# Kernel optimization log

Hardware: AMD Instinct MI355X
Metric: run time of the kernel (lower is better)

Reference implementation:

```python
import jax, jax.numpy as jnp
import numpy as np

B, S, D = 4, 2048, 1024
E = 16          # num_experts
K = 2           # num_experts_per_tok
F = 512         # moe_intermediate_size
FS = 2048       # shared_expert_intermediate_size


def setup_inputs() -> dict:
    key = jax.random.key(0)
    ks = jax.random.split(key, 9)
    s = 0.02
    return {
        "hidden_states": jax.random.normal(ks[0], (B, S, D), jnp.float32),
        "router_w": jax.random.normal(ks[1], (E, D), jnp.float32) * s,   # torch Linear-style [out,in]
        "Wg": jax.random.normal(ks[2], (E, D, F), jnp.float32) * s,      # gate_proj per expert
        "Wu": jax.random.normal(ks[3], (E, D, F), jnp.float32) * s,      # up_proj per expert
        "Wd": jax.random.normal(ks[4], (E, F, D), jnp.float32) * s,      # down_proj per expert
        "Sg": jax.random.normal(ks[5], (D, FS), jnp.float32) * s,        # shared expert gate_proj
        "Su": jax.random.normal(ks[6], (D, FS), jnp.float32) * s,        # shared expert up_proj
        "Sd": jax.random.normal(ks[7], (FS, D), jnp.float32) * s,        # shared expert down_proj
        "shared_gate_w": jax.random.normal(ks[8], (D, 1), jnp.float32) * s,
    }


def reference(hidden_states, router_w, Wg, Wu, Wd, Sg, Su, Sd, shared_gate_w):
    b, s, d = hidden_states.shape
    x = hidden_states.reshape(-1, d)                      # [T, D]
    T = x.shape[0]

    # --- router (Qwen3NextTopKRouter): fp32 softmax -> topk -> renorm ---
    logits = jnp.einsum("td,ed->te", x.astype(jnp.float32), router_w.astype(jnp.float32))
    probs = jax.nn.softmax(logits, axis=-1)               # [T, E]
    top_w, top_i = jax.lax.top_k(probs, K)                # [T, K]
    top_w = top_w / jnp.sum(top_w, axis=-1, keepdims=True)  # norm_topk_prob
    top_w = top_w.astype(x.dtype)

    # dense combine weights [T, E]: zero except at selected experts (index_add semantics)
    dense_w = jnp.zeros((T, E), x.dtype).at[jnp.arange(T)[:, None], top_i].add(top_w)

    # --- experts: SwiGLU per expert, scan over the fixed expert axis ---
    def body(acc, params):
        wg, wu, wd, cw = params                            # cw: [T]
        h = jax.nn.silu(x @ wg) * (x @ wu)                 # [T, F]
        return acc + cw[:, None] * (h @ wd), None

    expert_out, _ = jax.lax.scan(body, jnp.zeros_like(x), (Wg, Wu, Wd, dense_w.T))

    # --- shared expert with sigmoid gate ---
    shared = (jax.nn.silu(x @ Sg) * (x @ Su)) @ Sd         # [T, D]
    shared = jax.nn.sigmoid(x @ shared_gate_w) * shared

    out = expert_out + shared
    return out.reshape(b, s, d)
```

## Files before the change

kernel.cpp:

```cpp
#include <hip/hip_runtime.h>

typedef __attribute__((ext_vector_type(8))) short short8;
typedef __attribute__((ext_vector_type(4))) float f32x4;
typedef unsigned short u16;
typedef unsigned int u32;

#define DEVI __device__ __forceinline__

DEVI u16 f2b(float f) {
  u32 u = __float_as_uint(f);
  u32 r = u + 0x7FFFu + ((u >> 16) & 1u);
  return (u16)(r >> 16);
}
DEVI float b2f(u16 h) { return __uint_as_float(((u32)h) << 16); }
DEVI float silu(float g) { return g / (1.f + __expf(-g)); }

constexpr int T_ = 8192, D_ = 1024, E_ = 16, F_ = 512, FS_ = 2048;

constexpr size_t OFF_XB   = 0;
constexpr size_t OFF_WGU  = OFF_XB  + (size_t)T_ * D_ * 2;
constexpr size_t OFF_WDT  = OFF_WGU + (size_t)E_ * 2 * F_ * D_ * 2;
constexpr size_t OFF_SGU  = OFF_WDT + (size_t)E_ * D_ * F_ * 2;
constexpr size_t OFF_SDT  = OFF_SGU + (size_t)2 * FS_ * D_ * 2;
constexpr size_t OFF_HB   = OFF_SDT + (size_t)D_ * FS_ * 2;
constexpr size_t OFF_HS   = OFF_HB  + (size_t)2 * T_ * F_ * 2;
constexpr size_t OFF_PAIR = OFF_HS  + (size_t)T_ * FS_ * 2;
constexpr size_t OFF_PW   = OFF_PAIR + (size_t)2 * T_ * D_ * 2;
constexpr size_t OFF_GATE = OFF_PW  + (size_t)2 * T_ * 4;
constexpr size_t OFF_CNT  = OFF_GATE + (size_t)T_ * 4;
constexpr size_t OFF_TOP2 = OFF_CNT + 64;
constexpr size_t OFF_LIST = OFF_TOP2 + (size_t)T_ * 4;

__global__ void prep_kernel(
    const float4* __restrict__ x4, const float4* __restrict__ rw4,
    const float4* __restrict__ sgw4, int* __restrict__ top2e,
    float* __restrict__ pw, float* __restrict__ gate, ushort4* __restrict__ xb4,
    const float* __restrict__ Wg, const float* __restrict__ Wu, const float* __restrict__ Wd,
    const float* __restrict__ Sg, const float* __restrict__ Su, const float* __restrict__ Sd,
    u16* __restrict__ wgu, u16* __restrict__ wdT,
    u16* __restrict__ sgu, u16* __restrict__ sdT) {
  const int tid = threadIdx.x;
  const int bid = blockIdx.x;
  if (bid >= 7680) {
    const int lane = tid & 63, wid = tid >> 6;
    const int t = (bid - 7680) * 4 + wid;
    const float4* xr = x4 + (size_t)t * (D_ / 4);
    float acc[17];
#pragma unroll
    for (int e = 0; e < 17; ++e) acc[e] = 0.f;
    ushort4 xo[4];
#pragma unroll
    for (int j = 0; j < 4; ++j) {
      const int d4 = j * 64 + lane;
      float4 xv = xr[d4];
      xo[j] = make_ushort4(f2b(xv.x), f2b(xv.y), f2b(xv.z), f2b(xv.w));
#pragma unroll
      for (int e = 0; e < 16; ++e) {
        float4 wv = rw4[e * 256 + d4];
        acc[e] = fmaf(xv.x, wv.x, fmaf(xv.y, wv.y, fmaf(xv.z, wv.z, fmaf(xv.w, wv.w, acc[e]))));
      }
      float4 sv = sgw4[d4];
      acc[16] = fmaf(xv.x, sv.x, fmaf(xv.y, sv.y, fmaf(xv.z, sv.z, fmaf(xv.w, sv.w, acc[16]))));
    }
#pragma unroll
    for (int j = 0; j < 4; ++j)
      xb4[(size_t)t * 256 + j * 64 + lane] = xo[j];
#pragma unroll
    for (int e = 0; e < 17; ++e) {
      float v = acc[e];
#pragma unroll
      for (int off = 32; off; off >>= 1) v += __shfl_xor(v, off);
      acc[e] = v;
    }
    if (lane == 0) {
      int i1 = 0; float l1 = acc[0];
#pragma unroll
      for (int e = 1; e < 16; ++e) if (acc[e] > l1) { l1 = acc[e]; i1 = e; }
      int i2 = (i1 == 0) ? 1 : 0; float l2 = acc[i2];
#pragma unroll
      for (int e = 0; e < 16; ++e) {
        if (e == i1) continue;
        if (acc[e] > l2) { l2 = acc[e]; i2 = e; }
      }
      float w1 = 1.f / (1.f + expf(l2 - l1));
      top2e[t] = i1 | (i2 << 8);
      pw[2 * t] = w1;
      pw[2 * t + 1] = 1.f - w1;
      gate[t] = 1.f / (1.f + expf(-acc[16]));
    }
    return;
  }
  __shared__ float lds[64][65];
  int i = bid;
  const float* in; u16* out; int R, C, mode, rem;
  if (i < 6144) {
    int j = i >> 11; rem = i & 2047;
    int b = rem >> 7; rem &= 127;
    if (j == 0)      { in = Wg + (size_t)b * D_ * F_; out = wgu + (size_t)b * 2 * F_ * D_; R = D_; C = F_;  mode = 0; }
    else if (j == 1) { in = Wu + (size_t)b * D_ * F_; out = wgu + (size_t)b * 2 * F_ * D_; R = D_; C = F_;  mode = 1; }
    else             { in = Wd + (size_t)b * F_ * D_; out = wdT + (size_t)b * D_ * F_;     R = F_; C = D_;  mode = 2; }
  } else {
    int r2 = i - 6144; int j = r2 >> 9; rem = r2 & 511;
    if (j == 0)      { in = Sg; out = sgu; R = D_;  C = FS_; mode = 0; }
    else if (j == 1) { in = Su; out = sgu; R = D_;  C = FS_; mode = 1; }
    else             { in = Sd; out = sdT; R = FS_; C = D_;  mode = 2; }
  }
  const int ntx = C >> 6;
  const int cx = rem % ntx, cy = rem / ntx;
  const int c0 = cx * 64, r0 = cy * 64;
  {
    const int tx4 = (tid & 15) * 4, ty = tid >> 4;
#pragma unroll
    for (int p = 0; p < 4; ++p) {
      const int rr = ty + p * 16;
      float4 v = *(const float4*)&in[(size_t)(r0 + rr) * C + c0 + tx4];
      lds[rr][tx4] = v.x; lds[rr][tx4 + 1] = v.y; lds[rr][tx4 + 2] = v.z; lds[rr][tx4 + 3] = v.w;
    }
  }
  __syncthreads();
  {
    const int ol = tid >> 2, seg = tid & 3;
    const int f = c0 + ol;
    size_t orow;
    if (mode == 2) orow = f;
    else orow = (size_t)((f >> 4) << 5) + (f & 15) + (mode == 1 ? 16 : 0);
    u16 vals[16];
#pragma unroll
    for (int k = 0; k < 16; ++k) vals[k] = f2b(lds[seg * 16 + k][ol]);
    u16* dst = out + orow * R + r0 + seg * 16;
    *(short8*)dst = *(short8*)&vals[0];
    *(short8*)(dst + 8) = *(short8*)&vals[8];
  }
}

__global__ __launch_bounds__(1024) void compact_kernel(
    const int* __restrict__ top2e, int* __restrict__ lists, int* __restrict__ counts) {
  const int e = blockIdx.x;
  const int tid = threadIdx.x, lane = tid & 63, wid = tid >> 6;
  __shared__ int wsum[16];
  __shared__ int base;
  if (tid == 0) base = 0;
  __syncthreads();
  for (int c0 = 0; c0 < T_; c0 += 1024) {
    const int t = c0 + tid;
    const int pk = top2e[t];
    int slot = -1;
    if ((pk & 0xFF) == e) slot = 2 * t;
    else if (((pk >> 8) & 0xFF) == e) slot = 2 * t + 1;
    const unsigned long long m = __ballot(slot >= 0);
    const int myofs = __popcll(m & ((1ULL << lane) - 1ULL));
    if (lane == 0) wsum[wid] = __popcll(m);
    __syncthreads();
    const int b = base;
    int wbase = 0;
#pragma unroll
    for (int w = 0; w < 16; ++w) if (w < wid) wbase += wsum[w];
    if (slot >= 0) lists[e * T_ + b + wbase + myofs] = slot;
    __syncthreads();
    if (tid == 0) {
      int s = 0;
#pragma unroll
      for (int w = 0; w < 16; ++w) s += wsum[w];
      base += s;
    }
    __syncthreads();
  }
  if (tid == 0) counts[e] = base;
}

DEVI void gl_lds16(const void* gsrc, void* lds) {
  __builtin_amdgcn_global_load_lds((const __attribute__((address_space(1))) unsigned int*)gsrc,
                                   (__attribute__((address_space(3))) unsigned int*)lds, 16, 0, 0);
}

DEVI void prefix16(const int* counts, int e, int& cnt, int& roff) {
  cnt = counts[e];
  int s = 0;
#pragma unroll
  for (int k = 0; k < E_; ++k) s += (k < e) ? counts[k] : 0;
  roff = s;
}

__global__ __launch_bounds__(256, 2) void gu_gemm(
    const u16* __restrict__ xb, const u16* __restrict__ wgu, const u16* __restrict__ sgu,
    u16* __restrict__ hb, u16* __restrict__ hs,
    const int* __restrict__ counts, const int* __restrict__ lists) {
  extern __shared__ char smem[];
  const int tid = threadIdx.x;
  const int bid = blockIdx.x;
  const bool se = (bid >= 2048);
  int mt, nt, e = 0, cnt = 0, roff = 0;
  const u16* B0;
  if (!se) {
    e = bid >> 7; int r = bid & 127; mt = r >> 3; nt = r & 7;
    prefix16(counts, e, cnt, roff);
    if (mt * 128 >= cnt) return;
    B0 = wgu + (size_t)e * 2 * F_ * D_;
  } else {
    int st = bid - 2048;
    mt = st & 63; nt = st >> 6;
    B0 = sgu;
  }

  const int lane = tid & 63, wid = tid >> 6;
  const int wm = wid >> 1, wn = wid & 1;
  const int lr = lane & 15, lg = lane >> 4;
  const int ldsrow = tid >> 3;
  const int kslot = (tid & 7) << 4;
  constexpr size_t strideB = (size_t)D_ * 2;
  const char* aSrc[4]; const char* bSrc[4];
#pragma unroll
  for (int q = 0; q < 4; ++q) {
    int row = q * 32 + ldsrow;
    int kb = kslot ^ ((row & 7) << 4);
    int r = mt * 128 + row;
    long arow;
    if (!se) arow = (r < cnt) ? (lists[e * T_ + r] >> 1) : 0;
    else arow = r;
    aSrc[q] = (const char*)xb + (size_t)arow * strideB + kb;
    int nrow = nt * 128 + row;
    bSrc[q] = (const char*)B0 + (size_t)nrow * strideB + kb;
  }

  const f32x4 fz = {0.f, 0.f, 0.f, 0.f};
  f32x4 acc[4][4];
#pragma unroll
  for (int i = 0; i < 4; ++i)
#pragma unroll
    for (int j = 0; j < 4; ++j) acc[i][j] = fz;

  const int sw = (lr & 7) << 4;
  constexpr int nks = D_ / 64;

  {
    char* dst = smem;
#pragma unroll
    for (int q = 0; q < 4; ++q) gl_lds16(aSrc[q], dst + q * 4096 + tid * 16);
#pragma unroll
    for (int q = 0; q < 4; ++q) gl_lds16(bSrc[q], dst + 16384 + q * 4096 + tid * 16);
  }
  __syncthreads();

  int cur = 0;
  for (int ks = 0; ks < nks; ++ks) {
    if (ks + 1 < nks) {
      const int kbo = (ks + 1) * 128;
      char* dst = smem + (cur ^ 1) * 32768;
#pragma unroll
      for (int q = 0; q < 4; ++q) gl_lds16(aSrc[q] + kbo, dst + q * 4096 + tid * 16);
#pragma unroll
      for (int q = 0; q < 4; ++q) gl_lds16(bSrc[q] + kbo, dst + 16384 + q * 4096 + tid * 16);
    }
    const char* As = smem + cur * 32768;
    const char* Bs = As + 16384;
#pragma unroll
    for (int kk = 0; kk < 2; ++kk) {
      const int ko = kk * 64 + lg * 16;
      short8 af[4];
#pragma unroll
      for (int fm = 0; fm < 4; ++fm) {
        int row = wm * 64 + fm * 16 + lr;
        af[fm] = *(const short8*)(As + row * 128 + (ko ^ sw));
      }
#pragma unroll
      for (int fn = 0; fn < 4; ++fn) {
        int col = wn * 64 + fn * 16 + lr;
        short8 bf = *(const short8*)(Bs + col * 128 + (ko ^ sw));
#pragma unroll
        for (int fm = 0; fm < 4; ++fm)
          acc[fm][fn] = __builtin_amdgcn_mfma_f32_16x16x32_bf16(af[fm], bf, acc[fm][fn], 0, 0, 0);
      }
    }
    __syncthreads();
    cur ^= 1;
  }

  const int c0 = 16 * (4 * nt + 2 * wn);
  const int r0 = mt * 128;
#pragma unroll
  for (int fm = 0; fm < 4; ++fm) {
#pragma unroll
    for (int j = 0; j < 4; ++j) {
      const int r = r0 + wm * 64 + fm * 16 + lg * 4 + j;
      if (!se && r >= cnt) continue;
      float h0 = silu(acc[fm][0][j]) * acc[fm][1][j];
      float h1 = silu(acc[fm][2][j]) * acc[fm][3][j];
      if (!se) {
        hb[(size_t)(roff + r) * F_ + c0 + lr] = f2b(h0);
        hb[(size_t)(roff + r) * F_ + c0 + 16 + lr] = f2b(h1);
      } else {
        hs[(size_t)r * FS_ + c0 + lr] = f2b(h0);
        hs[(size_t)r * FS_ + c0 + 16 + lr] = f2b(h1);
      }
    }
  }
}

template <int MODE>
__global__ __launch_bounds__(256, 2) void moe_gemm(
    const u16* __restrict__ Abase, const u16* __restrict__ B0,
    u16* __restrict__ outb, float* __restrict__ outf,
    const int* __restrict__ counts, const int* __restrict__ lists,
    const float* __restrict__ pw, const float* __restrict__ gate,
    const u16* __restrict__ pairb, int Kdim) {
  extern __shared__ char smem[];
  const int tid = threadIdx.x;
  const int mt = blockIdx.x, nt = blockIdx.y, e = blockIdx.z;

  int cnt = 0;
  const u16* A = Abase;
  if constexpr (MODE == 1) {
    int roff;
    prefix16(counts, e, cnt, roff);
    if (mt * 128 >= cnt) return;
    A = Abase + (size_t)roff * Kdim;
    B0 += (size_t)e * D_ * F_;
  }

  const int lane = tid & 63, wid = tid >> 6;
  const int wm = wid >> 1, wn = wid & 1;
  const int lr = lane & 15, lg = lane >> 4;
  const int ldsrow = tid >> 3;
  const int kslot = (tid & 7) << 4;
  const size_t strideB = (size_t)Kdim * 2;
  const char* aSrc[4]; const char* bSrc[4];
#pragma unroll
  for (int q = 0; q < 4; ++q) {
    int row = q * 32 + ldsrow;
    int kb = kslot ^ ((row & 7) << 4);
    long arow;
    if constexpr (MODE == 1) {
      int r = mt * 128 + row;
      arow = (r < cnt) ? r : (cnt - 1);
    } else {
      arow = mt * 128 + row;
    }
    aSrc[q] = (const char*)A + (size_t)arow * strideB + kb;
    int nrow = nt * 128 + row;
    bSrc[q] = (const char*)B0 + (size_t)nrow * strideB + kb;
  }

  const f32x4 fz = {0.f, 0.f, 0.f, 0.f};
  f32x4 acc[4][4];
#pragma unroll
  for (int i = 0; i < 4; ++i)
#pragma unroll
    for (int j = 0; j < 4; ++j) acc[i][j] = fz;

  const int nks = Kdim >> 6;
  const int sw = (lr & 7) << 4;

  {
    char* dst = smem;
#pragma unroll
    for (int q = 0; q < 4; ++q) gl_lds16(aSrc[q], dst + q * 4096 + tid * 16);
#pragma unroll
    for (int q = 0; q < 4; ++q) gl_lds16(bSrc[q], dst + 16384 + q * 4096 + tid * 16);
  }
  __syncthreads();

  int cur = 0;
  for (int ks = 0; ks < nks; ++ks) {
    if (ks + 1 < nks) {
      const int kbo = (ks + 1) * 128;
      char* dst = smem + (cur ^ 1) * 32768;
#pragma unroll
      for (int q = 0; q < 4; ++q) gl_lds16(aSrc[q] + kbo, dst + q * 4096 + tid * 16);
#pragma unroll
      for (int q = 0; q < 4; ++q) gl_lds16(bSrc[q] + kbo, dst + 16384 + q * 4096 + tid * 16);
    }
    const char* As = smem + cur * 32768;
    const char* Bs = As + 16384;
#pragma unroll
    for (int kk = 0; kk < 2; ++kk) {
      const int ko = kk * 64 + lg * 16;
      short8 af[4];
#pragma unroll
      for (int fm = 0; fm < 4; ++fm) {
        int row = wm * 64 + fm * 16 + lr;
        af[fm] = *(const short8*)(As + row * 128 + (ko ^ sw));
      }
#pragma unroll
      for (int fn = 0; fn < 4; ++fn) {
        int col = wn * 64 + fn * 16 + lr;
        short8 bf = *(const short8*)(Bs + col * 128 + (ko ^ sw));
#pragma unroll
        for (int fm = 0; fm < 4; ++fm)
          acc[fm][fn] = __builtin_amdgcn_mfma_f32_16x16x32_bf16(af[fm], bf, acc[fm][fn], 0, 0, 0);
      }
    }
    __syncthreads();
    cur ^= 1;
  }

  const int r0 = mt * 128;
#pragma unroll
  for (int fm = 0; fm < 4; ++fm) {
#pragma unroll
    for (int j = 0; j < 4; ++j) {
      const int rowt = wm * 64 + fm * 16 + lg * 4 + j;
      const int r = r0 + rowt;
      if constexpr (MODE == 1) {
        if (r >= cnt) continue;
      }
      int slot = 0;
      float rsc = 0.f;
      if constexpr (MODE == 1) { slot = lists[e * T_ + r]; rsc = pw[slot]; }
      if constexpr (MODE == 3) rsc = gate[r];
#pragma unroll
      for (int fn = 0; fn < 4; ++fn) {
        const int c = nt * 128 + wn * 64 + fn * 16 + lr;
        float v = acc[fm][fn][j];
        if constexpr (MODE == 1) {
          outb[(size_t)slot * D_ + c] = f2b(rsc * v);
        } else {
          float o = v * rsc + b2f(pairb[(size_t)(2 * r) * D_ + c]) + b2f(pairb[(size_t)(2 * r + 1) * D_ + c]);
          outf[(size_t)r * D_ + c] = o;
        }
      }
    }
  }
}

extern "C" void kernel_launch(void* const* d_in, const int* in_sizes, int n_in,
                              void* d_out, int out_size, void* d_ws, size_t ws_size,
                              hipStream_t stream) {
  const float* x   = (const float*)d_in[0];
  const float* rw  = (const float*)d_in[1];
  const float* Wg  = (const float*)d_in[2];
  const float* Wu  = (const float*)d_in[3];
  const float* Wd  = (const float*)d_in[4];
  const float* Sg  = (const float*)d_in[5];
  const float* Su  = (const float*)d_in[6];
  const float* Sd  = (const float*)d_in[7];
  const float* sgw = (const float*)d_in[8];
  float* out = (float*)d_out;

  unsigned char* ws = (unsigned char*)d_ws;
  u16* xb    = (u16*)(ws + OFF_XB);
  u16* wgu   = (u16*)(ws + OFF_WGU);
  u16* wdT   = (u16*)(ws + OFF_WDT);
  u16* sgu   = (u16*)(ws + OFF_SGU);
  u16* sdT   = (u16*)(ws + OFF_SDT);
  u16* hb    = (u16*)(ws + OFF_HB);
  u16* hs    = (u16*)(ws + OFF_HS);
  u16* pairb = (u16*)(ws + OFF_PAIR);
  float* pwf   = (float*)(ws + OFF_PW);
  float* gatef = (float*)(ws + OFF_GATE);
  int* cnti    = (int*)(ws + OFF_CNT);
  int* top2i   = (int*)(ws + OFF_TOP2);
  int* listsi  = (int*)(ws + OFF_LIST);

  prep_kernel<<<9728, 256, 0, stream>>>(
      (const float4*)x, (const float4*)rw, (const float4*)sgw,
      top2i, pwf, gatef, (ushort4*)xb,
      Wg, Wu, Wd, Sg, Su, Sd, wgu, wdT, sgu, sdT);
  compact_kernel<<<E_, 1024, 0, stream>>>(top2i, listsi, cnti);

  gu_gemm<<<4096, 256, 65536, stream>>>(xb, wgu, sgu, hb, hs, cnti, listsi);
  moe_gemm<1><<<dim3(16, 8, 16), 256, 65536, stream>>>(hb, wdT, pairb, nullptr,
                                                       cnti, listsi, pwf, gatef, nullptr, 512);
  moe_gemm<3><<<dim3(64, 8, 1), 256, 65536, stream>>>(hs, sdT, nullptr, out,
                                                      cnti, listsi, pwf, gatef, pairb, 2048);

  (void)in_sizes; (void)n_in; (void)out_size; (void)ws_size;
}
```

Baseline: 290.0 us.

## Load A fragments directly to registers, stage only B in LDS, raise occupancy

The GEMM kernels no longer stage the A tile through LDS. Each wave loads its A fragments straight from global memory into registers, double-buffered across two register sets, while only the B tile goes through LDS via global_load_lds. Halving the LDS footprint to 32KB lets launch bounds rise to 3 blocks per CU. The cost is that A rows are now read redundantly by the two waves sharing an M slice, global loads are less coalesced (16-byte per lane at gathered rows), and register pressure is higher.

```diff
diff --git a/kernel.cpp b/kernel.cpp
--- a/kernel.cpp
+++ b/kernel.cpp
@@ -181,7 +181,48 @@
   roff = s;
 }
 
-__global__ __launch_bounds__(256, 2) void gu_gemm(
+#define LOAD_A(dst, ksv)                                                     \
+  _Pragma("unroll")                                                          \
+  for (int fm = 0; fm < 4; ++fm) {                                           \
+    dst[fm][0] = *(const short8*)(aRow[fm] + (ksv) * 128);                   \
+    dst[fm][1] = *(const short8*)(aRow[fm] + (ksv) * 128 + 64);              \
+  }
+
+#define STAGE_B(buf, ksv)                                                    \
+  _Pragma("unroll")                                                          \
+  for (int q = 0; q < 4; ++q) gl_lds16(bSrc[q] + (ksv) * 128, (buf) + q * 4096 + tid * 16);
+
+#define COMPUTE(buf, af)                                                     \
+  _Pragma("unroll")                                                          \
+  for (int kk = 0; kk < 2; ++kk) {                                           \
+    const int ko = kk * 64 + lg * 16;                                        \
+    _Pragma("unroll")                                                        \
+    for (int fn = 0; fn < 4; ++fn) {                                         \
+      int col = wn * 64 + fn * 16 + lr;                                      \
+      short8 bf = *(const short8*)((buf) + col * 128 + (ko ^ sw));           \
+      _Pragma("unroll")                                                      \
+      for (int fm = 0; fm < 4; ++fm)                                         \
+        acc[fm][fn] = __builtin_amdgcn_mfma_f32_16x16x32_bf16(af[fm][kk], bf, acc[fm][fn], 0, 0, 0); \
+    }                                                                        \
+  }
+
+#define KLOOP(NKS)                                                           \
+  short8 afA[4][2], afB[4][2];                                               \
+  LOAD_A(afA, 0);                                                            \
+  STAGE_B(smem, 0);                                                          \
+  __syncthreads();                                                           \
+  for (int ks = 0; ks < (NKS); ks += 2) {                                    \
+    if (ks + 1 < (NKS)) { STAGE_B(smem + 16384, ks + 1); LOAD_A(afB, ks + 1); } \
+    COMPUTE(smem, afA);                                                      \
+    __syncthreads();                                                         \
+    if (ks + 1 < (NKS)) {                                                    \
+      if (ks + 2 < (NKS)) { STAGE_B(smem, ks + 2); LOAD_A(afA, ks + 2); }    \
+      COMPUTE(smem + 16384, afB);                                            \
+      __syncthreads();                                                       \
+    }                                                                        \
+  }
+
+__global__ __launch_bounds__(256, 3) void gu_gemm(
     const u16* __restrict__ xb, const u16* __restrict__ wgu, const u16* __restrict__ sgu,
     u16* __restrict__ hb, u16* __restrict__ hs,
     const int* __restrict__ counts, const int* __restrict__ lists) {
@@ -205,21 +246,27 @@
   const int lane = tid & 63, wid = tid >> 6;
   const int wm = wid >> 1, wn = wid & 1;
   const int lr = lane & 15, lg = lane >> 4;
+  const int sw = (lr & 7) << 4;
+  constexpr size_t strideB = (size_t)D_ * 2;
+
   const int ldsrow = tid >> 3;
   const int kslot = (tid & 7) << 4;
-  constexpr size_t strideB = (size_t)D_ * 2;
-  const char* aSrc[4]; const char* bSrc[4];
+  const char* bSrc[4];
 #pragma unroll
   for (int q = 0; q < 4; ++q) {
     int row = q * 32 + ldsrow;
     int kb = kslot ^ ((row & 7) << 4);
-    int r = mt * 128 + row;
+    bSrc[q] = (const char*)B0 + (size_t)(nt * 128 + row) * strideB + kb;
+  }
+
+  const char* aRow[4];
+#pragma unroll
+  for (int fm = 0; fm < 4; ++fm) {
+    int r = mt * 128 + wm * 64 + fm * 16 + lr;
     long arow;
     if (!se) arow = (r < cnt) ? (lists[e * T_ + r] >> 1) : 0;
     else arow = r;
-    aSrc[q] = (const char*)xb + (size_t)arow * strideB + kb;
-    int nrow = nt * 128 + row;
-    bSrc[q] = (const char*)B0 + (size_t)nrow * strideB + kb;
+    aRow[fm] = (const char*)xb + (size_t)arow * strideB + lg * 16;
   }
 
   const f32x4 fz = {0.f, 0.f, 0.f, 0.f};
@@ -229,51 +276,7 @@
 #pragma unroll
     for (int j = 0; j < 4; ++j) acc[i][j] = fz;
 
-  const int sw = (lr & 7) << 4;
-  constexpr int nks = D_ / 64;
-
-  {
-    char* dst = smem;
-#pragma unroll
-    for (int q = 0; q < 4; ++q) gl_lds16(aSrc[q], dst + q * 4096 + tid * 16);
-#pragma unroll
-    for (int q = 0; q < 4; ++q) gl_lds16(bSrc[q], dst + 16384 + q * 4096 + tid * 16);
-  }
-  __syncthreads();
-
-  int cur = 0;
-  for (int ks = 0; ks < nks; ++ks) {
-    if (ks + 1 < nks) {
-      const int kbo = (ks + 1) * 128;
-      char* dst = smem + (cur ^ 1) * 32768;
-#pragma unroll
-      for (int q = 0; q < 4; ++q) gl_lds16(aSrc[q] + kbo, dst + q * 4096 + tid * 16);
-#pragma unroll
-      for (int q = 0; q < 4; ++q) gl_lds16(bSrc[q] + kbo, dst + 16384 + q * 4096 + tid * 16);
-    }
-    const char* As = smem + cur * 32768;
-    const char* Bs = As + 16384;
-#pragma unroll
-    for (int kk = 0; kk < 2; ++kk) {
-      const int ko = kk * 64 + lg * 16;
-      short8 af[4];
-#pragma unroll
-      for (int fm = 0; fm < 4; ++fm) {
-        int row = wm * 64 + fm * 16 + lr;
-        af[fm] = *(const short8*)(As + row * 128 + (ko ^ sw));
-      }
-#pragma unroll
-      for (int fn = 0; fn < 4; ++fn) {
-        int col = wn * 64 + fn * 16 + lr;
-        short8 bf = *(const short8*)(Bs + col * 128 + (ko ^ sw));
-#pragma unroll
-        for (int fm = 0; fm < 4; ++fm)
-          acc[fm][fn] = __builtin_amdgcn_mfma_f32_16x16x32_bf16(af[fm], bf, acc[fm][fn], 0, 0, 0);
-      }
-    }
-    __syncthreads();
-    cur ^= 1;
-  }
+  KLOOP(16);
 
   const int c0 = 16 * (4 * nt + 2 * wn);
   const int r0 = mt * 128;
@@ -297,7 +300,7 @@
 }
 
 template <int MODE>
-__global__ __launch_bounds__(256, 2) void moe_gemm(
+__global__ __launch_bounds__(256, 3) void moe_gemm(
     const u16* __restrict__ Abase, const u16* __restrict__ B0,
     u16* __restrict__ outb, float* __restrict__ outf,
     const int* __restrict__ counts, const int* __restrict__ lists,
@@ -320,24 +323,27 @@
   const int lane = tid & 63, wid = tid >> 6;
   const int wm = wid >> 1, wn = wid & 1;
   const int lr = lane & 15, lg = lane >> 4;
+  const int sw = (lr & 7) << 4;
+  const size_t strideB = (size_t)Kdim * 2;
+
   const int ldsrow = tid >> 3;
   const int kslot = (tid & 7) << 4;
-  const size_t strideB = (size_t)Kdim * 2;
-  const char* aSrc[4]; const char* bSrc[4];
+  const char* bSrc[4];
 #pragma unroll
   for (int q = 0; q < 4; ++q) {
     int row = q * 32 + ldsrow;
     int kb = kslot ^ ((row & 7) << 4);
+    bSrc[q] = (const char*)B0 + (size_t)(nt * 128 + row) * strideB + kb;
+  }
+
+  const char* aRow[4];
+#pragma unroll
+  for (int fm = 0; fm < 4; ++fm) {
+    int r = mt * 128 + wm * 64 + fm * 16 + lr;
     long arow;
-    if constexpr (MODE == 1) {
-      int r = mt * 128 + row;
-      arow = (r < cnt) ? r : (cnt - 1);
-    } else {
-      arow = mt * 128 + row;
-    }
-    aSrc[q] = (const char*)A + (size_t)arow * strideB + kb;
-    int nrow = nt * 128 + row;
-    bSrc[q] = (const char*)B0 + (size_t)nrow * strideB + kb;
+    if constexpr (MODE == 1) arow = (r < cnt) ? r : (cnt - 1);
+    else arow = r;
+    aRow[fm] = (const char*)A + (size_t)arow * strideB + lg * 16;
   }
 
   const f32x4 fz = {0.f, 0.f, 0.f, 0.f};
@@ -348,50 +354,7 @@
     for (int j = 0; j < 4; ++j) acc[i][j] = fz;
 
   const int nks = Kdim >> 6;
-  const int sw = (lr & 7) << 4;
-
-  {
-    char* dst = smem;
-#pragma unroll
-    for (int q = 0; q < 4; ++q) gl_lds16(aSrc[q], dst + q * 4096 + tid * 16);
-#pragma unroll
-    for (int q = 0; q < 4; ++q) gl_lds16(bSrc[q], dst + 16384 + q * 4096 + tid * 16);
-  }
-  __syncthreads();
-
-  int cur = 0;
-  for (int ks = 0; ks < nks; ++ks) {
-    if (ks + 1 < nks) {
-      const int kbo = (ks + 1) * 128;
-      char* dst = smem + (cur ^ 1) * 32768;
-#pragma unroll
-      for (int q = 0; q < 4; ++q) gl_lds16(aSrc[q] + kbo, dst + q * 4096 + tid * 16);
-#pragma unroll
-      for (int q = 0; q < 4; ++q) gl_lds16(bSrc[q] + kbo, dst + 16384 + q * 4096 + tid * 16);
-    }
-    const char* As = smem + cur * 32768;
-    const char* Bs = As + 16384;
-#pragma unroll
-    for (int kk = 0; kk < 2; ++kk) {
-      const int ko = kk * 64 + lg * 16;
-      short8 af[4];
-#pragma unroll
-      for (int fm = 0; fm < 4; ++fm) {
-        int row = wm * 64 + fm * 16 + lr;
-        af[fm] = *(const short8*)(As + row * 128 + (ko ^ sw));
-      }
-#pragma unroll
-      for (int fn = 0; fn < 4; ++fn) {
-        int col = wn * 64 + fn * 16 + lr;
-        short8 bf = *(const short8*)(Bs + col * 128 + (ko ^ sw));
-#pragma unroll
-        for (int fm = 0; fm < 4; ++fm)
-          acc[fm][fn] = __builtin_amdgcn_mfma_f32_16x16x32_bf16(af[fm], bf, acc[fm][fn], 0, 0, 0);
-      }
-    }
-    __syncthreads();
-    cur ^= 1;
-  }
+  KLOOP(nks);
 
   const int r0 = mt * 128;
 #pragma unroll
@@ -457,10 +420,10 @@
       Wg, Wu, Wd, Sg, Su, Sd, wgu, wdT, sgu, sdT);
   compact_kernel<<<E_, 1024, 0, stream>>>(top2i, listsi, cnti);
 
-  gu_gemm<<<4096, 256, 65536, stream>>>(xb, wgu, sgu, hb, hs, cnti, listsi);
-  moe_gemm<1><<<dim3(16, 8, 16), 256, 65536, stream>>>(hb, wdT, pairb, nullptr,
+  gu_gemm<<<4096, 256, 32768, stream>>>(xb, wgu, sgu, hb, hs, cnti, listsi);
+  moe_gemm<1><<<dim3(16, 8, 16), 256, 32768, stream>>>(hb, wdT, pairb, nullptr,
                                                        cnti, listsi, pwf, gatef, nullptr, 512);
-  moe_gemm<3><<<dim3(64, 8, 1), 256, 65536, stream>>>(hs, sdT, nullptr, out,
+  moe_gemm<3><<<dim3(64, 8, 1), 256, 32768, stream>>>(hs, sdT, nullptr, out,
                                                       cnti, listsi, pwf, gatef, pairb, 2048);
 
   (void)in_sizes; (void)n_in; (void)out_size; (void)ws_size;
```

After: 473.8 us. 63.4% more time.

## Drop LDS double buffering to single buffer and raise occupancy to four blocks

Applied to the files above, without the earlier changes.

Replaces the double-buffered global-to-LDS prefetch in all three GEMM kernels with a single 32KB buffer that is loaded, synchronised, consumed and synchronised again on every k-step. Shared memory per block is halved and launch bounds are raised to allow four resident blocks per CU. The aim is to hide memory latency through more concurrent blocks instead of in-block prefetch. The cost is that loads no longer overlap compute within a block, and tighter register limits could cause spills.

```diff
diff --git a/kernel.cpp b/kernel.cpp
--- a/kernel.cpp
+++ b/kernel.cpp
@@ -181,7 +181,7 @@
   roff = s;
 }
 
-__global__ __launch_bounds__(256, 2) void gu_gemm(
+__global__ __launch_bounds__(256, 4) void gu_gemm(
     const u16* __restrict__ xb, const u16* __restrict__ wgu, const u16* __restrict__ sgu,
     u16* __restrict__ hb, u16* __restrict__ hs,
     const int* __restrict__ counts, const int* __restrict__ lists) {
@@ -232,27 +232,15 @@
   const int sw = (lr & 7) << 4;
   constexpr int nks = D_ / 64;
 
-  {
-    char* dst = smem;
-#pragma unroll
-    for (int q = 0; q < 4; ++q) gl_lds16(aSrc[q], dst + q * 4096 + tid * 16);
-#pragma unroll
-    for (int q = 0; q < 4; ++q) gl_lds16(bSrc[q], dst + 16384 + q * 4096 + tid * 16);
-  }
-  __syncthreads();
-
-  int cur = 0;
   for (int ks = 0; ks < nks; ++ks) {
-    if (ks + 1 < nks) {
-      const int kbo = (ks + 1) * 128;
-      char* dst = smem + (cur ^ 1) * 32768;
-#pragma unroll
-      for (int q = 0; q < 4; ++q) gl_lds16(aSrc[q] + kbo, dst + q * 4096 + tid * 16);
-#pragma unroll
-      for (int q = 0; q < 4; ++q) gl_lds16(bSrc[q] + kbo, dst + 16384 + q * 4096 + tid * 16);
-    }
-    const char* As = smem + cur * 32768;
-    const char* Bs = As + 16384;
+    const int kbo = ks * 128;
+#pragma unroll
+    for (int q = 0; q < 4; ++q) gl_lds16(aSrc[q] + kbo, smem + q * 4096 + tid * 16);
+#pragma unroll
+    for (int q = 0; q < 4; ++q) gl_lds16(bSrc[q] + kbo, smem + 16384 + q * 4096 + tid * 16);
+    __syncthreads();
+    const char* As = smem;
+    const char* Bs = smem + 16384;
 #pragma unroll
     for (int kk = 0; kk < 2; ++kk) {
       const int ko = kk * 64 + lg * 16;
@@ -272,7 +260,6 @@
       }
     }
     __syncthreads();
-    cur ^= 1;
   }
 
   const int c0 = 16 * (4 * nt + 2 * wn);
@@ -297,7 +284,7 @@
 }
 
 template <int MODE>
-__global__ __launch_bounds__(256, 2) void moe_gemm(
+__global__ __launch_bounds__(256, 4) void moe_gemm(
     const u16* __restrict__ Abase, const u16* __restrict__ B0,
     u16* __restrict__ outb, float* __restrict__ outf,
     const int* __restrict__ counts, const int* __restrict__ lists,
@@ -350,27 +337,15 @@
   const int nks = Kdim >> 6;
   const int sw = (lr & 7) << 4;
 
-  {
-    char* dst = smem;
-#pragma unroll
-    for (int q = 0; q < 4; ++q) gl_lds16(aSrc[q], dst + q * 4096 + tid * 16);
-#pragma unroll
-    for (int q = 0; q < 4; ++q) gl_lds16(bSrc[q], dst + 16384 + q * 4096 + tid * 16);
-  }
-  __syncthreads();
-
-  int cur = 0;
   for (int ks = 0; ks < nks; ++ks) {
-    if (ks + 1 < nks) {
-      const int kbo = (ks + 1) * 128;
-      char* dst = smem + (cur ^ 1) * 32768;
-#pragma unroll
-      for (int q = 0; q < 4; ++q) gl_lds16(aSrc[q] + kbo, dst + q * 4096 + tid * 16);
-#pragma unroll
-      for (int q = 0; q < 4; ++q) gl_lds16(bSrc[q] + kbo, dst + 16384 + q * 4096 + tid * 16);
-    }
-    const char* As = smem + cur * 32768;
-    const char* Bs = As + 16384;
+    const int kbo = ks * 128;
+#pragma unroll
+    for (int q = 0; q < 4; ++q) gl_lds16(aSrc[q] + kbo, smem + q * 4096 + tid * 16);
+#pragma unroll
+    for (int q = 0; q < 4; ++q) gl_lds16(bSrc[q] + kbo, smem + 16384 + q * 4096 + tid * 16);
+    __syncthreads();
+    const char* As = smem;
+    const char* Bs = smem + 16384;
 #pragma unroll
     for (int kk = 0; kk < 2; ++kk) {
       const int ko = kk * 64 + lg * 16;
@@ -390,7 +365,6 @@
       }
     }
     __syncthreads();
-    cur ^= 1;
   }
 
   const int r0 = mt * 128;
@@ -457,10 +431,10 @@
       Wg, Wu, Wd, Sg, Su, Sd, wgu, wdT, sgu, sdT);
   compact_kernel<<<E_, 1024, 0, stream>>>(top2i, listsi, cnti);
 
-  gu_gemm<<<4096, 256, 65536, stream>>>(xb, wgu, sgu, hb, hs, cnti, listsi);
-  moe_gemm<1><<<dim3(16, 8, 16), 256, 65536, stream>>>(hb, wdT, pairb, nullptr,
+  gu_gemm<<<4096, 256, 32768, stream>>>(xb, wgu, sgu, hb, hs, cnti, listsi);
+  moe_gemm<1><<<dim3(16, 8, 16), 256, 32768, stream>>>(hb, wdT, pairb, nullptr,
                                                        cnti, listsi, pwf, gatef, nullptr, 512);
-  moe_gemm<3><<<dim3(64, 8, 1), 256, 65536, stream>>>(hs, sdT, nullptr, out,
+  moe_gemm<3><<<dim3(64, 8, 1), 256, 32768, stream>>>(hs, sdT, nullptr, out,
                                                       cnti, listsi, pwf, gatef, pairb, 2048);
 
   (void)in_sizes; (void)n_in; (void)out_size; (void)ws_size;
```

Measured after the change: 273.3 us. 1.06x faster.
